# Optimization experiments

Hardware: AMD Instinct MI355X
Metric: run time of the kernel (lower is better)

The kernel has to match this reference:

```python
import jax, jax.numpy as jnp
import numpy as np

LATENT = 1024
TEXT = 768
HEADS = 16
HEAD_DIM = LATENT // HEADS
SCALE = HEAD_DIM ** -0.5
LN_EPS = 1e-5


def setup_inputs() -> dict:
    key = jax.random.key(0)
    ks = jax.random.split(key, 16)
    B, Tx, Txf = 4, 4096, 256
    def lin(k, fan_in, fan_out):
        bound = 1.0 / np.sqrt(fan_in)
        kw, kb = jax.random.split(k)
        W = jax.random.uniform(kw, (fan_in, fan_out), jnp.float32, -bound, bound)
        b = jax.random.uniform(kb, (fan_out,), jnp.float32, -bound, bound)
        return W, b
    Wq, bq = lin(ks[0], LATENT, LATENT)
    Wk, bk = lin(ks[1], TEXT, LATENT)
    Wv, bv = lin(ks[2], TEXT, LATENT)
    Wo, bo = lin(ks[3], LATENT, LATENT)
    W1, b1 = lin(ks[4], LATENT, 4 * LATENT)
    W2, b2 = lin(ks[5], 4 * LATENT, LATENT)
    return {
        "x": jax.random.normal(ks[6], (B, Tx, LATENT), jnp.float32),
        "xf": jax.random.normal(ks[7], (B, Txf, TEXT), jnp.float32),
        "Wq": Wq, "bq": bq, "Wk": Wk, "bk": bk, "Wv": Wv, "bv": bv,
        "Wo": Wo, "bo": bo,
        "ln_g": jnp.ones((LATENT,), jnp.float32),
        "ln_b": jnp.zeros((LATENT,), jnp.float32),
        "W1": W1, "b1": b1, "W2": W2, "b2": b2,
    }


def reference(x, xf, Wq, bq, Wk, bk, Wv, bv, Wo, bo, ln_g, ln_b, W1, b1, W2, b2):
    B, Tx, D = x.shape
    Txf = xf.shape[1]
    # projections -> [B, H, T, Dh]
    q = (x @ Wq + bq).reshape(B, Tx, HEADS, HEAD_DIM).transpose(0, 2, 1, 3)
    k = (xf @ Wk + bk).reshape(B, Txf, HEADS, HEAD_DIM).transpose(0, 2, 1, 3)
    v = (xf @ Wv + bv).reshape(B, Txf, HEADS, HEAD_DIM).transpose(0, 2, 1, 3)
    # chunked loop in original == full softmax over keys (dropout=0 at eval)
    scores = jnp.einsum('bhqd,bhkd->bhqk', q * SCALE, k)
    probs = jax.nn.softmax(scores, axis=-1)
    attn = jnp.einsum('bhqk,bhkd->bhqd', probs, v)
    out = attn.transpose(0, 2, 1, 3).reshape(B, Tx, D)
    out = out @ Wo + bo
    # FFN: LayerNorm -> Linear -> GELU(exact) -> Linear
    mu = jnp.mean(out, axis=-1, keepdims=True)
    var = jnp.var(out, axis=-1, keepdims=True)
    h = (out - mu) * jax.lax.rsqrt(var + LN_EPS) * ln_g + ln_b
    h = jax.nn.gelu(h @ W1 + b1, approximate=False)
    ffn = h @ W2 + b2
    out = out + ffn
    return x + out
```

## Files before the change

### kernel.cpp

```cpp
#include <hip/hip_runtime.h>
#include <hip/hip_bf16.h>
#include <cmath>

typedef __bf16 bf16_t;
typedef __bf16 bf16x8 __attribute__((ext_vector_type(8)));
typedef __bf16 bf16x4 __attribute__((ext_vector_type(4)));
typedef float f32x4 __attribute__((ext_vector_type(4)));

#define LATENT 1024
#define HEADS 16
#define HD 64
#define TX 4096
#define TXF 256
#define SCALE_ATTN 0.125f

static __device__ __forceinline__ float b2f(bf16_t b) { return (float)b; }
static __device__ __forceinline__ bf16_t f2b(float f) { return (bf16_t)f; }

static __device__ __forceinline__ void glds16(const bf16_t* g, bf16_t* l) {
    __builtin_amdgcn_global_load_lds(
        (const __attribute__((address_space(1))) void*)g,
        (__attribute__((address_space(3))) void*)l, 16, 0, 0);
}

#define MFMA16(a, b, c) __builtin_amdgcn_mfma_f32_16x16x32_bf16(a, b, c, 0, 0, 0)

__global__ __launch_bounds__(256) void cvt_k(const float* __restrict__ in,
                                             bf16_t* __restrict__ out, long n4) {
    long i = (long)blockIdx.x * 256 + threadIdx.x;
    long stride = (long)gridDim.x * 256;
    for (; i < n4; i += stride) {
        float4 v = ((const float4*)in)[i];
        bf16x4 o;
        o[0] = f2b(v.x); o[1] = f2b(v.y); o[2] = f2b(v.z); o[3] = f2b(v.w);
        *(bf16x4*)&out[i * 4] = o;
    }
}

__global__ __launch_bounds__(256) void tr_k(const float* __restrict__ in,
                                            bf16_t* __restrict__ out,
                                            int R, int C) {
    __shared__ float t[32][33];
    int bx = blockIdx.x, by = blockIdx.y;
    int x = threadIdx.x & 31, y0 = threadIdx.x >> 5;
    for (int i = 0; i < 32; i += 8)
        t[y0 + i][x] = in[(long)(by * 32 + y0 + i) * C + bx * 32 + x];
    __syncthreads();
    for (int i = 0; i < 32; i += 8)
        out[(long)(bx * 32 + y0 + i) * R + by * 32 + x] = f2b(t[x][y0 + i]);
}

template <int EPI>
__global__ __launch_bounds__(256, 2) void gemm_k(
    const bf16_t* __restrict__ A, const bf16_t* __restrict__ Bt,
    const float* __restrict__ bias, void* __restrict__ C,
    const bf16_t* __restrict__ resb16, const float* __restrict__ resf32,
    int M, int N, int K) {
    __shared__ __align__(16) bf16_t As[128 * 64];
    __shared__ __align__(16) bf16_t Bs[128 * 64];
    int tid = threadIdx.x;
    int lane = tid & 63, wid = tid >> 6;
    int quad = lane >> 4, l16 = lane & 15;
    int wm = wid >> 1, wn = wid & 1;
    int srow0 = wid * 8 + (lane >> 3);
    int schunk = (lane & 7) ^ (lane >> 3);

    f32x4 acc[4][4] = {};
    long bm = blockIdx.x, bn = blockIdx.y;
    const bf16_t* Ab = A + (bm * 128 + srow0) * (long)K + schunk * 8;
    const bf16_t* Bb = Bt + (bn * 128 + srow0) * (long)K + schunk * 8;
    bf16_t* AsD = As + wid * 512;
    bf16_t* BsD = Bs + wid * 512;

    for (int k0 = 0; k0 < K; k0 += 64) {
        __syncthreads();
#pragma unroll
        for (int t = 0; t < 4; t++) {
            glds16(Ab + k0 + (long)t * 32 * K, AsD + t * 2048);
            glds16(Bb + k0 + (long)t * 32 * K, BsD + t * 2048);
        }
        __syncthreads();
#pragma unroll
        for (int s = 0; s < 2; s++) {
            bf16x8 af[4], bfr[4];
#pragma unroll
            for (int mi = 0; mi < 4; mi++) {
                int r = wm * 64 + mi * 16 + l16;
                af[mi] = *(const bf16x8*)&As[r * 64 + (((s * 4 + quad) ^ (r & 7)) * 8)];
            }
#pragma unroll
            for (int ni = 0; ni < 4; ni++) {
                int r = wn * 64 + ni * 16 + l16;
                bfr[ni] = *(const bf16x8*)&Bs[r * 64 + (((s * 4 + quad) ^ (r & 7)) * 8)];
            }
#pragma unroll
            for (int mi = 0; mi < 4; mi++)
#pragma unroll
                for (int ni = 0; ni < 4; ni++)
                    acc[mi][ni] = MFMA16(af[mi], bfr[ni], acc[mi][ni]);
        }
    }

    int colb = (int)bn * 128 + wn * 64;
    float bvv[4];
#pragma unroll
    for (int ni = 0; ni < 4; ni++) bvv[ni] = bias[colb + ni * 16 + l16];
#pragma unroll
    for (int mi = 0; mi < 4; mi++) {
        long grow = bm * 128 + wm * 64 + mi * 16 + quad * 4;
#pragma unroll
        for (int r = 0; r < 4; r++) {
            long ro = (grow + r) * (long)N;
#pragma unroll
            for (int ni = 0; ni < 4; ni++) {
                long idx = ro + colb + ni * 16 + l16;
                float v = acc[mi][ni][r] + bvv[ni];
                if (EPI == 0) {
                    ((bf16_t*)C)[idx] = f2b(v);
                } else if (EPI == 2) {
                    ((bf16_t*)C)[idx] =
                        f2b(0.5f * v * (1.0f + erff(v * 0.70710678118f)));
                } else {
                    ((float*)C)[idx] = v + b2f(resb16[idx]) + resf32[idx];
                }
            }
        }
    }
}

template <int EPI>
__global__ __launch_bounds__(512, 2) void gemm256_k(
    const bf16_t* __restrict__ A, const bf16_t* __restrict__ Bt,
    const float* __restrict__ bias, void* __restrict__ C,
    const bf16_t* __restrict__ resb16, const float* __restrict__ resf32,
    int M, int N, int K) {
    __shared__ __align__(16) bf16_t As[2 * 16384];
    __shared__ __align__(16) bf16_t Bs[2 * 16384];
    int tid = threadIdx.x;
    int lane = tid & 63, wid = tid >> 6;
    int quad = lane >> 4, l16 = lane & 15;
    int wm = wid >> 2, wn = wid & 3;
    long bm = blockIdx.x, bn = blockIdx.y;
    int NT = K >> 6;

    int srow = wid * 8 + (lane >> 3);
    int schunk = ((lane & 7) ^ (lane >> 3)) * 8;
    const bf16_t* Asrc = A + (bm * 256 + srow) * (long)K + schunk;
    const bf16_t* Bsrc = Bt + (bn * 256 + srow) * (long)K + schunk;

    auto stageA = [&](int t, int r) {
        glds16(Asrc + ((long)t * 64 + (long)r * 64 * K),
               As + ((t & 1) * 16384 + r * 4096 + wid * 512));
    };
    auto stageB = [&](int t, int r) {
        glds16(Bsrc + ((long)t * 64 + (long)r * 64 * K),
               Bs + ((t & 1) * 16384 + r * 4096 + wid * 512));
    };

    stageA(0, 0); stageA(0, 1); stageA(0, 2); stageA(0, 3);
    stageB(0, 0); stageB(0, 1); stageB(0, 2); stageB(0, 3);
    stageA(1, 0); stageA(1, 1); stageA(1, 2); stageA(1, 3);
    f32x4 acc[8][4] = {};
    bf16x8 af[4][2], bq0[2][2], bq1[2][2];
    asm volatile("s_waitcnt vmcnt(4)" ::: "memory");
    __builtin_amdgcn_s_barrier();

    for (int t = 0; t < NT; ++t) {
        int cur = t & 1;
        const bf16_t* AL = As + cur * 16384;
        const bf16_t* BL = Bs + cur * 16384;
#pragma unroll
        for (int mi = 0; mi < 4; ++mi) {
            int r = wm * 128 + mi * 16 + l16;
            af[mi][0] = *(const bf16x8*)&AL[r * 64 + ((quad ^ (r & 7)) * 8)];
            af[mi][1] = *(const bf16x8*)&AL[r * 64 + (((4 + quad) ^ (r & 7)) * 8)];
        }
#pragma unroll
        for (int ni = 0; ni < 2; ++ni) {
            int r = wn * 64 + ni * 16 + l16;
            bq0[ni][0] = *(const bf16x8*)&BL[r * 64 + ((quad ^ (r & 7)) * 8)];
            bq0[ni][1] = *(const bf16x8*)&BL[r * 64 + (((4 + quad) ^ (r & 7)) * 8)];
        }
        if (t + 1 < NT) { stageB(t + 1, 0); stageB(t + 1, 1); }
        __builtin_amdgcn_s_barrier();
        __builtin_amdgcn_s_setprio(1);
#pragma unroll
        for (int mi = 0; mi < 4; ++mi)
#pragma unroll
            for (int ni = 0; ni < 2; ++ni) {
                acc[mi][ni] = MFMA16(af[mi][0], bq0[ni][0], acc[mi][ni]);
                acc[mi][ni] = MFMA16(af[mi][1], bq0[ni][1], acc[mi][ni]);
            }
        __builtin_amdgcn_s_setprio(0);
        __builtin_amdgcn_s_barrier();
#pragma unroll
        for (int ni = 0; ni < 2; ++ni) {
            int r = wn * 64 + 32 + ni * 16 + l16;
            bq1[ni][0] = *(const bf16x8*)&BL[r * 64 + ((quad ^ (r & 7)) * 8)];
            bq1[ni][1] = *(const bf16x8*)&BL[r * 64 + (((4 + quad) ^ (r & 7)) * 8)];
        }
        if (t + 2 < NT) { stageA(t + 2, 0); stageA(t + 2, 2); }
        __builtin_amdgcn_s_barrier();
        __builtin_amdgcn_s_setprio(1);
#pragma unroll
        for (int mi = 0; mi < 4; ++mi)
#pragma unroll
            for (int ni = 0; ni < 2; ++ni) {
                acc[mi][2 + ni] = MFMA16(af[mi][0], bq1[ni][0], acc[mi][2 + ni]);
                acc[mi][2 + ni] = MFMA16(af[mi][1], bq1[ni][1], acc[mi][2 + ni]);
            }
        __builtin_amdgcn_s_setprio(0);
        __builtin_amdgcn_s_barrier();
#pragma unroll
        for (int mi = 0; mi < 4; ++mi) {
            int r = wm * 128 + 64 + mi * 16 + l16;
            af[mi][0] = *(const bf16x8*)&AL[r * 64 + ((quad ^ (r & 7)) * 8)];
            af[mi][1] = *(const bf16x8*)&AL[r * 64 + (((4 + quad) ^ (r & 7)) * 8)];
        }
        if (t + 1 < NT) { stageB(t + 1, 2); stageB(t + 1, 3); }
        __builtin_amdgcn_s_barrier();
        __builtin_amdgcn_s_setprio(1);
#pragma unroll
        for (int mi = 0; mi < 4; ++mi)
#pragma unroll
            for (int ni = 0; ni < 2; ++ni) {
                acc[4 + mi][ni] = MFMA16(af[mi][0], bq0[ni][0], acc[4 + mi][ni]);
                acc[4 + mi][ni] = MFMA16(af[mi][1], bq0[ni][1], acc[4 + mi][ni]);
            }
        __builtin_amdgcn_s_setprio(0);
        __builtin_amdgcn_s_barrier();
        if (t + 2 < NT) { stageA(t + 2, 1); stageA(t + 2, 3); }
        __builtin_amdgcn_s_barrier();
        __builtin_amdgcn_s_setprio(1);
#pragma unroll
        for (int mi = 0; mi < 4; ++mi)
#pragma unroll
            for (int ni = 0; ni < 2; ++ni) {
                acc[4 + mi][2 + ni] = MFMA16(af[mi][0], bq1[ni][0], acc[4 + mi][2 + ni]);
                acc[4 + mi][2 + ni] = MFMA16(af[mi][1], bq1[ni][1], acc[4 + mi][2 + ni]);
            }
        __builtin_amdgcn_s_setprio(0);
        if (t + 2 < NT) {
            asm volatile("s_waitcnt vmcnt(2)" ::: "memory");
        } else if (t + 1 < NT) {
            asm volatile("s_waitcnt vmcnt(0)" ::: "memory");
        }
        __builtin_amdgcn_s_barrier();
    }

    int colb = (int)bn * 256 + wn * 64;
    float bvv[4];
#pragma unroll
    for (int ni = 0; ni < 4; ++ni) bvv[ni] = bias[colb + ni * 16 + l16];
#pragma unroll
    for (int mi = 0; mi < 8; ++mi) {
        long grow = bm * 256 + wm * 128 + mi * 16 + quad * 4;
#pragma unroll
        for (int r = 0; r < 4; ++r) {
            long ro = (grow + r) * (long)N;
#pragma unroll
            for (int ni = 0; ni < 4; ++ni) {
                long idx = ro + colb + ni * 16 + l16;
                float v = acc[mi][ni][r] + bvv[ni];
                if (EPI == 0) {
                    ((bf16_t*)C)[idx] = f2b(v);
                } else if (EPI == 2) {
                    ((bf16_t*)C)[idx] =
                        f2b(0.5f * v * (1.0f + erff(v * 0.70710678118f)));
                } else {
                    ((float*)C)[idx] = v + b2f(resb16[idx]) + resf32[idx];
                }
            }
        }
    }
}

__global__ __launch_bounds__(256, 2) void attn_k(const bf16_t* __restrict__ Q,
                                                 const bf16_t* __restrict__ Kb,
                                                 const bf16_t* __restrict__ Vb,
                                                 bf16_t* __restrict__ Ob) {
    __shared__ __align__(16) bf16_t SM[32768];
    bf16_t* Ks = SM;
    bf16_t* Vt = SM + 16384;
    int tid = threadIdx.x;
    int lane = tid & 63, w = tid >> 6;
    int quad = lane >> 4, l16 = lane & 15;
    int qt = blockIdx.x & 63;
    int bh = blockIdx.x >> 6;
    int b = bh >> 4, h = bh & 15;

    {
        const uint4* ks = (const uint4*)(Kb + ((long)(b * TXF + tid) * LATENT + h * HD));
#pragma unroll
        for (int cc = 0; cc < 8; cc++)
            *(uint4*)&Ks[tid * 64 + ((cc ^ (tid & 7)) * 8)] = ks[cc];
        const uint4* vs = (const uint4*)(Vb + ((long)(b * TXF + tid) * LATENT + h * HD));
#pragma unroll
        for (int cc = 0; cc < 8; cc++) {
            uint4 v = vs[cc];
            const bf16_t* e = (const bf16_t*)&v;
#pragma unroll
            for (int j = 0; j < 8; j++) {
                int d = cc * 8 + j;
                Vt[d * 256 + (((tid >> 3) ^ (d & 7)) * 8) + (tid & 7)] = e[j];
            }
        }
    }
    long qrow = (long)(b * TX + qt * 64 + w * 16 + l16) * LATENT + h * HD;
    bf16x8 aq0 = *(const bf16x8*)(Q + qrow + quad * 8);
    bf16x8 aq1 = *(const bf16x8*)(Q + qrow + 32 + quad * 8);
    __syncthreads();

    f32x4 sacc[16] = {};
#pragma unroll
    for (int ni = 0; ni < 16; ni++) {
        int kr = ni * 16 + l16;
        bf16x8 b0 = *(const bf16x8*)&Ks[kr * 64 + ((quad ^ (kr & 7)) * 8)];
        bf16x8 b1 = *(const bf16x8*)&Ks[kr * 64 + (((4 + quad) ^ (kr & 7)) * 8)];
        sacc[ni] = MFMA16(aq0, b0, sacc[ni]);
        sacc[ni] = MFMA16(aq1, b1, sacc[ni]);
    }
#pragma unroll
    for (int r = 0; r < 4; r++) {
        float m = -3e38f;
#pragma unroll
        for (int ni = 0; ni < 16; ni++) m = fmaxf(m, sacc[ni][r]);
#pragma unroll
        for (int off = 1; off < 16; off <<= 1) m = fmaxf(m, __shfl_xor(m, off, 64));
        float s = 0.f;
#pragma unroll
        for (int ni = 0; ni < 16; ni++) {
            float p = __expf((sacc[ni][r] - m) * SCALE_ATTN);
            sacc[ni][r] = p;
            s += p;
        }
#pragma unroll
        for (int off = 1; off < 16; off <<= 1) s += __shfl_xor(s, off, 64);
        float inv = 1.0f / s;
#pragma unroll
        for (int ni = 0; ni < 16; ni++) sacc[ni][r] *= inv;
    }
    __syncthreads();

    bf16_t* Ps = SM;
#pragma unroll
    for (int r = 0; r < 4; r++) {
        int row = w * 16 + quad * 4 + r;
#pragma unroll
        for (int ni = 0; ni < 16; ni++) {
            int col = ni * 16 + l16;
            Ps[row * 256 + (((col >> 3) ^ (row & 7)) * 8) + (col & 7)] =
                f2b(sacc[ni][r]);
        }
    }
    __syncthreads();

    f32x4 oacc[4] = {};
#pragma unroll
    for (int s = 0; s < 8; s++) {
        int prow = w * 16 + l16;
        bf16x8 ap = *(const bf16x8*)&Ps[prow * 256 + (((s * 4 + quad) ^ (prow & 7)) * 8)];
#pragma unroll
        for (int ni = 0; ni < 4; ni++) {
            int vr = ni * 16 + l16;
            bf16x8 bv = *(const bf16x8*)&Vt[vr * 256 + (((s * 4 + quad) ^ (vr & 7)) * 8)];
            oacc[ni] = MFMA16(ap, bv, oacc[ni]);
        }
    }
#pragma unroll
    for (int r = 0; r < 4; r++) {
        long orow = (long)(b * TX + qt * 64 + w * 16 + quad * 4 + r) * LATENT + h * HD;
#pragma unroll
        for (int ni = 0; ni < 4; ni++)
            Ob[orow + ni * 16 + l16] = f2b(oacc[ni][r]);
    }
}

__global__ __launch_bounds__(256) void ln_k(const bf16_t* __restrict__ O,
                                            const float* __restrict__ g,
                                            const float* __restrict__ bb,
                                            bf16_t* __restrict__ H) {
    long row = blockIdx.x;
    int c = threadIdx.x * 4;
    bf16x4 v = *(const bf16x4*)(O + row * LATENT + c);
    float vv[4] = {b2f(v[0]), b2f(v[1]), b2f(v[2]), b2f(v[3])};
    float s = vv[0] + vv[1] + vv[2] + vv[3];
    float s2 = vv[0] * vv[0] + vv[1] * vv[1] + vv[2] * vv[2] + vv[3] * vv[3];
#pragma unroll
    for (int off = 1; off < 64; off <<= 1) {
        s += __shfl_xor(s, off, 64);
        s2 += __shfl_xor(s2, off, 64);
    }
    __shared__ float red[8];
    int lane = threadIdx.x & 63, w = threadIdx.x >> 6;
    if (lane == 0) { red[w] = s; red[w + 4] = s2; }
    __syncthreads();
    s = red[0] + red[1] + red[2] + red[3];
    s2 = red[4] + red[5] + red[6] + red[7];
    float mu = s * (1.0f / 1024.0f);
    float var = s2 * (1.0f / 1024.0f) - mu * mu;
    float rstd = rsqrtf(var + 1e-5f);
    bf16_t* out = H + row * LATENT + c;
#pragma unroll
    for (int j = 0; j < 4; j++)
        out[j] = f2b((vv[j] - mu) * rstd * g[c + j] + bb[c + j]);
}

extern "C" void kernel_launch(void* const* d_in, const int* in_sizes, int n_in,
                              void* d_out, int out_size, void* d_ws,
                              size_t ws_size, hipStream_t stream) {
    const float* x = (const float*)d_in[0];
    const float* xf = (const float*)d_in[1];
    const float* Wq = (const float*)d_in[2];
    const float* bq = (const float*)d_in[3];
    const float* Wk = (const float*)d_in[4];
    const float* bk = (const float*)d_in[5];
    const float* Wv = (const float*)d_in[6];
    const float* bv = (const float*)d_in[7];
    const float* Wo = (const float*)d_in[8];
    const float* bo = (const float*)d_in[9];
    const float* lng = (const float*)d_in[10];
    const float* lnb = (const float*)d_in[11];
    const float* W1 = (const float*)d_in[12];
    const float* b1 = (const float*)d_in[13];
    const float* W2 = (const float*)d_in[14];
    const float* b2 = (const float*)d_in[15];

    char* ws = (char*)d_ws;
    size_t off = 0;
    auto alloc = [&](size_t bytes) {
        void* p = ws + off;
        off += (bytes + 255) & ~(size_t)255;
        return p;
    };
    bf16_t* WqT = (bf16_t*)alloc((size_t)1024 * 1024 * 2);
    bf16_t* WkT = (bf16_t*)alloc((size_t)1024 * 768 * 2);
    bf16_t* WvT = (bf16_t*)alloc((size_t)1024 * 768 * 2);
    bf16_t* WoT = (bf16_t*)alloc((size_t)1024 * 1024 * 2);
    bf16_t* W1T = (bf16_t*)alloc((size_t)4096 * 1024 * 2);
    bf16_t* W2T = (bf16_t*)alloc((size_t)1024 * 4096 * 2);
    bf16_t* Obuf = (bf16_t*)alloc((size_t)16384 * 1024 * 2);
    bf16_t* Hbuf = (bf16_t*)alloc((size_t)16384 * 1024 * 2);
    size_t transient0 = off;
    bf16_t* xc = (bf16_t*)alloc((size_t)16384 * 1024 * 2);
    bf16_t* xfc = (bf16_t*)alloc((size_t)1024 * 768 * 2);
    bf16_t* Qbuf = (bf16_t*)alloc((size_t)16384 * 1024 * 2);
    bf16_t* Kbuf = (bf16_t*)alloc((size_t)1024 * 1024 * 2);
    bf16_t* Vbuf = (bf16_t*)alloc((size_t)1024 * 1024 * 2);
    bf16_t* Abuf = (bf16_t*)alloc((size_t)16384 * 1024 * 2);
    bf16_t* H1 = (bf16_t*)(ws + transient0);

    dim3 blk(256), blk5(512);
    cvt_k<<<dim3(4096), blk, 0, stream>>>(x, xc, (long)16384 * 1024 / 4);
    cvt_k<<<dim3(768), blk, 0, stream>>>(xf, xfc, (long)1024 * 768 / 4);
    tr_k<<<dim3(32, 32), blk, 0, stream>>>(Wq, WqT, 1024, 1024);
    tr_k<<<dim3(32, 24), blk, 0, stream>>>(Wk, WkT, 768, 1024);
    tr_k<<<dim3(32, 24), blk, 0, stream>>>(Wv, WvT, 768, 1024);
    tr_k<<<dim3(32, 32), blk, 0, stream>>>(Wo, WoT, 1024, 1024);
    tr_k<<<dim3(128, 32), blk, 0, stream>>>(W1, W1T, 1024, 4096);
    tr_k<<<dim3(32, 128), blk, 0, stream>>>(W2, W2T, 4096, 1024);

    gemm256_k<0><<<dim3(64, 4), blk5, 0, stream>>>(xc, WqT, bq, Qbuf, nullptr, nullptr, 16384, 1024, 1024);
    gemm_k<0><<<dim3(8, 8), blk, 0, stream>>>(xfc, WkT, bk, Kbuf, nullptr, nullptr, 1024, 1024, 768);
    gemm_k<0><<<dim3(8, 8), blk, 0, stream>>>(xfc, WvT, bv, Vbuf, nullptr, nullptr, 1024, 1024, 768);
    attn_k<<<dim3(4096), blk, 0, stream>>>(Qbuf, Kbuf, Vbuf, Abuf);
    gemm256_k<0><<<dim3(64, 4), blk5, 0, stream>>>(Abuf, WoT, bo, Obuf, nullptr, nullptr, 16384, 1024, 1024);
    ln_k<<<dim3(16384), blk, 0, stream>>>(Obuf, lng, lnb, Hbuf);
    gemm256_k<2><<<dim3(64, 16), blk5, 0, stream>>>(Hbuf, W1T, b1, H1, nullptr, nullptr, 16384, 4096, 1024);
    gemm256_k<3><<<dim3(64, 4), blk5, 0, stream>>>(H1, W2T, b2, d_out, Obuf, x, 16384, 1024, 4096);
}
```

Measured before the change: 679.8 us.

## Replace staggered 4-phase GEMM pipeline with simple ping-pong double buffering

The 256x256 GEMM main loop drops its interleaved schedule, in which A was prefetched two tiles ahead and B one tile ahead in quarter slices across four barrier-separated phases. It now uses two named LDS buffers in a ping-pong pattern. Each iteration loads all B fragments once, issues the next full A/B tile stage, runs two MFMA halves, then waits for all loads and hits a single barrier. This cuts barrier count and register-fragment juggling. In exchange it loses the deeper prefetch distance and the fine-grained overlap, so the vmcnt(0) wait each iteration may expose global-load latency.

```diff
diff --git a/kernel.cpp b/kernel.cpp
--- a/kernel.cpp
+++ b/kernel.cpp
@@ -134,8 +134,10 @@
     const float* __restrict__ bias, void* __restrict__ C,
     const bf16_t* __restrict__ resb16, const float* __restrict__ resf32,
     int M, int N, int K) {
-    __shared__ __align__(16) bf16_t As[2 * 16384];
-    __shared__ __align__(16) bf16_t Bs[2 * 16384];
+    __shared__ __align__(16) bf16_t As0[16384];
+    __shared__ __align__(16) bf16_t As1[16384];
+    __shared__ __align__(16) bf16_t Bs0[16384];
+    __shared__ __align__(16) bf16_t Bs1[16384];
     int tid = threadIdx.x;
     int lane = tid & 63, wid = tid >> 6;
     int quad = lane >> 4, l16 = lane & 15;
@@ -148,104 +150,74 @@
     const bf16_t* Asrc = A + (bm * 256 + srow) * (long)K + schunk;
     const bf16_t* Bsrc = Bt + (bn * 256 + srow) * (long)K + schunk;
 
-    auto stageA = [&](int t, int r) {
-        glds16(Asrc + ((long)t * 64 + (long)r * 64 * K),
-               As + ((t & 1) * 16384 + r * 4096 + wid * 512));
+    auto stage = [&](bf16_t* Ad, bf16_t* Bd, int t) {
+#pragma unroll
+        for (int r = 0; r < 4; ++r)
+            glds16(Asrc + ((long)t * 64 + (long)r * 64 * K),
+                   Ad + r * 4096 + wid * 512);
+#pragma unroll
+        for (int r = 0; r < 4; ++r)
+            glds16(Bsrc + ((long)t * 64 + (long)r * 64 * K),
+                   Bd + r * 4096 + wid * 512);
     };
-    auto stageB = [&](int t, int r) {
-        glds16(Bsrc + ((long)t * 64 + (long)r * 64 * K),
-               Bs + ((t & 1) * 16384 + r * 4096 + wid * 512));
-    };
-
-    stageA(0, 0); stageA(0, 1); stageA(0, 2); stageA(0, 3);
-    stageB(0, 0); stageB(0, 1); stageB(0, 2); stageB(0, 3);
-    stageA(1, 0); stageA(1, 1); stageA(1, 2); stageA(1, 3);
+
     f32x4 acc[8][4] = {};
-    bf16x8 af[4][2], bq0[2][2], bq1[2][2];
-    asm volatile("s_waitcnt vmcnt(4)" ::: "memory");
-    __builtin_amdgcn_s_barrier();
-
-    for (int t = 0; t < NT; ++t) {
-        int cur = t & 1;
-        const bf16_t* AL = As + cur * 16384;
-        const bf16_t* BL = Bs + cur * 16384;
+    bf16x8 af0[4][2], af1[4][2], bq[4][2];
+
+    auto loadA = [&](const bf16_t* AL, int half, bf16x8 (&af)[4][2]) {
 #pragma unroll
         for (int mi = 0; mi < 4; ++mi) {
-            int r = wm * 128 + mi * 16 + l16;
+            int r = wm * 128 + half * 64 + mi * 16 + l16;
             af[mi][0] = *(const bf16x8*)&AL[r * 64 + ((quad ^ (r & 7)) * 8)];
             af[mi][1] = *(const bf16x8*)&AL[r * 64 + (((4 + quad) ^ (r & 7)) * 8)];
         }
-#pragma unroll
-        for (int ni = 0; ni < 2; ++ni) {
+    };
+    auto loadB = [&](const bf16_t* BL) {
+#pragma unroll
+        for (int ni = 0; ni < 4; ++ni) {
             int r = wn * 64 + ni * 16 + l16;
-            bq0[ni][0] = *(const bf16x8*)&BL[r * 64 + ((quad ^ (r & 7)) * 8)];
-            bq0[ni][1] = *(const bf16x8*)&BL[r * 64 + (((4 + quad) ^ (r & 7)) * 8)];
-        }
-        if (t + 1 < NT) { stageB(t + 1, 0); stageB(t + 1, 1); }
+            bq[ni][0] = *(const bf16x8*)&BL[r * 64 + ((quad ^ (r & 7)) * 8)];
+            bq[ni][1] = *(const bf16x8*)&BL[r * 64 + (((4 + quad) ^ (r & 7)) * 8)];
+        }
+    };
+    auto mfmaHalf = [&](int half, bf16x8 (&af)[4][2]) {
+        __builtin_amdgcn_s_setprio(1);
+#pragma unroll
+        for (int mi = 0; mi < 4; ++mi)
+#pragma unroll
+            for (int ni = 0; ni < 4; ++ni) {
+                acc[half * 4 + mi][ni] =
+                    MFMA16(af[mi][0], bq[ni][0], acc[half * 4 + mi][ni]);
+                acc[half * 4 + mi][ni] =
+                    MFMA16(af[mi][1], bq[ni][1], acc[half * 4 + mi][ni]);
+            }
+        __builtin_amdgcn_s_setprio(0);
+    };
+
+    stage(As0, Bs0, 0);
+    asm volatile("s_waitcnt vmcnt(0)" ::: "memory");
+    __builtin_amdgcn_s_barrier();
+
+    int t = 0;
+    while (true) {
+        loadA(As0, 0, af0);
+        loadB(Bs0);
+        if (t + 1 < NT) stage(As1, Bs1, t + 1);
+        mfmaHalf(0, af0);
+        loadA(As0, 1, af1);
+        mfmaHalf(1, af1);
+        asm volatile("s_waitcnt vmcnt(0)" ::: "memory");
         __builtin_amdgcn_s_barrier();
-        __builtin_amdgcn_s_setprio(1);
-#pragma unroll
-        for (int mi = 0; mi < 4; ++mi)
-#pragma unroll
-            for (int ni = 0; ni < 2; ++ni) {
-                acc[mi][ni] = MFMA16(af[mi][0], bq0[ni][0], acc[mi][ni]);
-                acc[mi][ni] = MFMA16(af[mi][1], bq0[ni][1], acc[mi][ni]);
-            }
-        __builtin_amdgcn_s_setprio(0);
+        if (++t >= NT) break;
+        loadA(As1, 0, af0);
+        loadB(Bs1);
+        if (t + 1 < NT) stage(As0, Bs0, t + 1);
+        mfmaHalf(0, af0);
+        loadA(As1, 1, af1);
+        mfmaHalf(1, af1);
+        asm volatile("s_waitcnt vmcnt(0)" ::: "memory");
         __builtin_amdgcn_s_barrier();
-#pragma unroll
-        for (int ni = 0; ni < 2; ++ni) {
-            int r = wn * 64 + 32 + ni * 16 + l16;
-            bq1[ni][0] = *(const bf16x8*)&BL[r * 64 + ((quad ^ (r & 7)) * 8)];
-            bq1[ni][1] = *(const bf16x8*)&BL[r * 64 + (((4 + quad) ^ (r & 7)) * 8)];
-        }
-        if (t + 2 < NT) { stageA(t + 2, 0); stageA(t + 2, 2); }
-        __builtin_amdgcn_s_barrier();
-        __builtin_amdgcn_s_setprio(1);
-#pragma unroll
-        for (int mi = 0; mi < 4; ++mi)
-#pragma unroll
-            for (int ni = 0; ni < 2; ++ni) {
-                acc[mi][2 + ni] = MFMA16(af[mi][0], bq1[ni][0], acc[mi][2 + ni]);
-                acc[mi][2 + ni] = MFMA16(af[mi][1], bq1[ni][1], acc[mi][2 + ni]);
-            }
-        __builtin_amdgcn_s_setprio(0);
-        __builtin_amdgcn_s_barrier();
-#pragma unroll
-        for (int mi = 0; mi < 4; ++mi) {
-            int r = wm * 128 + 64 + mi * 16 + l16;
-            af[mi][0] = *(const bf16x8*)&AL[r * 64 + ((quad ^ (r & 7)) * 8)];
-            af[mi][1] = *(const bf16x8*)&AL[r * 64 + (((4 + quad) ^ (r & 7)) * 8)];
-        }
-        if (t + 1 < NT) { stageB(t + 1, 2); stageB(t + 1, 3); }
-        __builtin_amdgcn_s_barrier();
-        __builtin_amdgcn_s_setprio(1);
-#pragma unroll
-        for (int mi = 0; mi < 4; ++mi)
-#pragma unroll
-            for (int ni = 0; ni < 2; ++ni) {
-                acc[4 + mi][ni] = MFMA16(af[mi][0], bq0[ni][0], acc[4 + mi][ni]);
-                acc[4 + mi][ni] = MFMA16(af[mi][1], bq0[ni][1], acc[4 + mi][ni]);
-            }
-        __builtin_amdgcn_s_setprio(0);
-        __builtin_amdgcn_s_barrier();
-        if (t + 2 < NT) { stageA(t + 2, 1); stageA(t + 2, 3); }
-        __builtin_amdgcn_s_barrier();
-        __builtin_amdgcn_s_setprio(1);
-#pragma unroll
-        for (int mi = 0; mi < 4; ++mi)
-#pragma unroll
-            for (int ni = 0; ni < 2; ++ni) {
-                acc[4 + mi][2 + ni] = MFMA16(af[mi][0], bq1[ni][0], acc[4 + mi][2 + ni]);
-                acc[4 + mi][2 + ni] = MFMA16(af[mi][1], bq1[ni][1], acc[4 + mi][2 + ni]);
-            }
-        __builtin_amdgcn_s_setprio(0);
-        if (t + 2 < NT) {
-            asm volatile("s_waitcnt vmcnt(2)" ::: "memory");
-        } else if (t + 1 < NT) {
-            asm volatile("s_waitcnt vmcnt(0)" ::: "memory");
-        }
-        __builtin_amdgcn_s_barrier();
+        if (++t >= NT) break;
     }
 
     int colb = (int)bn * 256 + wn * 64;
```

Result: slower. 2.086 ms (+206.9%).
